# Kernel tuning notes

Measured on AMD Instinct MI355X. Metric: run time of the kernel, lower is better.

The kernel has to match this reference:

```python
import jax, jax.numpy as jnp
import numpy as np

N = 500000
C = 128
G = 4096


def setup_inputs() -> dict:
    key = jax.random.key(0)
    ks = jax.random.split(key, 6)
    x = jax.random.normal(ks[0], (N, C), dtype=jnp.float32)
    proj_w = jax.random.normal(ks[1], (C, C), dtype=jnp.float32) * (1.0 / np.sqrt(C))
    proj_b = jax.random.normal(ks[2], (C,), dtype=jnp.float32) * 0.01
    score_w = jax.random.normal(ks[3], (1, C), dtype=jnp.float32) * (1.0 / np.sqrt(C))
    score_b = jax.random.normal(ks[4], (1,), dtype=jnp.float32) * 0.01
    batch = jnp.sort(jax.random.randint(ks[5], (N,), 0, G, dtype=jnp.int32))
    return {"x": x, "proj_w": proj_w, "proj_b": proj_b,
            "score_w": score_w, "score_b": score_b,
            "batch": batch, "num_graphs": G}


def reference(x, proj_w, proj_b, score_w, score_b, batch, num_graphs):
    # h = tanh(Linear(x)); s = Linear(h) -> [N]
    h = jnp.tanh(x @ proj_w.T + proj_b)
    s = (h @ score_w.T + score_b)[:, 0]  # [N]
    # segment softmax over nodes of each graph
    m = jax.ops.segment_max(s, batch, num_segments=num_graphs)  # [G]
    m = jnp.where(jnp.isfinite(m), m, 0.0)  # guard empty segments
    e = jnp.exp(s - m[batch])
    denom = jax.ops.segment_sum(e, batch, num_segments=num_graphs)  # [G]
    w = e / jnp.maximum(denom[batch], 1e-30)  # [N]
    # weighted scatter-sum of raw features
    pooled = jax.ops.segment_sum(x * w[:, None], batch, num_segments=num_graphs)  # [G, C]
    return pooled
```

## Files before the change

### kernel.cpp

```cpp
#include <hip/hip_runtime.h>
#include <hip/hip_bf16.h>
#include <float.h>
#include <math.h>

#define CDIM 128

typedef __attribute__((ext_vector_type(8))) short short8v;
typedef __attribute__((ext_vector_type(4))) short short4v;
typedef __attribute__((ext_vector_type(4))) float f32x4;

__device__ __forceinline__ short bf16b(float f) {
    __hip_bfloat16 h = __float2bfloat16(f);
    return __builtin_bit_cast(short, h);
}

__device__ __forceinline__ float tanh_fast(float y) {
    float e = __expf(2.0f * y);
    return 1.0f - 2.0f / (e + 1.0f);
}

__device__ __forceinline__ int lower_bound_i(const int* __restrict__ b, int n, int v) {
    int lo = 0, hi = n;
    while (lo < hi) { int mid = (lo + hi) >> 1; if (b[mid] < v) lo = mid + 1; else hi = mid; }
    return lo;
}

__global__ void seg_bounds_kernel(const int* __restrict__ batch, int N, int G,
                                  int* __restrict__ seg) {
    int g = blockIdx.x * blockDim.x + threadIdx.x;
    if (g < G) seg[g] = lower_bound_i(batch, N, g);
    if (g == 0) seg[G] = N;
}

__global__ void wconv_kernel(const float* __restrict__ proj_w, short* __restrict__ wfrag) {
    int tid = blockIdx.x * 256 + threadIdx.x;
    int f = tid >> 6, l = tid & 63;
    int c  = ((f >> 2) << 4) | (l & 15);
    int k0 = ((f & 3) << 5) | ((l >> 4) << 3);
    short8v v;
    #pragma unroll
    for (int j = 0; j < 8; ++j) v[j] = bf16b(proj_w[c * CDIM + k0 + j]);
    ((short8v*)wfrag)[tid] = v;
}

__launch_bounds__(256, 4)
__global__ void pool_kernel(const float* __restrict__ x,
                            const short* __restrict__ wfrag,
                            const float* __restrict__ proj_b,
                            const float* __restrict__ score_w,
                            const float* __restrict__ score_b,
                            const int* __restrict__ seg,
                            float* __restrict__ out,
                            int N) {
    __shared__ short XsB[64 * 128];
    __shared__ float ps[4 * 64];
    __shared__ float cs[64];
    __shared__ __align__(16) float red[8 * 128];
    __shared__ float bc[2];

    const int g = blockIdx.x;
    const int t = threadIdx.x;
    const int lane = t & 63;
    const int w = t >> 6;
    const int start = seg[g];
    const int cnt = seg[g + 1] - start;

    if (cnt <= 0) {
        if (t < CDIM) out[g * CDIM + t] = 0.0f;
        return;
    }

    short8v wf[2][4];
    {
        const short8v* wfg = (const short8v*)wfrag;
        #pragma unroll
        for (int j = 0; j < 2; ++j)
            #pragma unroll
            for (int ks = 0; ks < 4; ++ks)
                wf[j][ks] = wfg[((((w << 1) | j) << 2 | ks) << 6) | lane];
    }
    float swl[2], pbl[2];
    #pragma unroll
    for (int j = 0; j < 2; ++j) {
        swl[j] = score_w[(((w << 1) | j) << 4) + (lane & 15)];
        pbl[j] = proj_b[(((w << 1) | j) << 4) + (lane & 15)];
    }
    const float sb = score_b[0];

    const float4* __restrict__ x4 = (const float4*)x;
    const int g8 = t >> 5;
    const int c4 = t & 31;
    const int al = lane & 15, ah = lane >> 4;

    float m_run = -FLT_MAX, l_run = 0.0f;
    float4 pa = make_float4(0.f, 0.f, 0.f, 0.f);

    for (int cb = 0; cb < cnt; cb += 64) {
        const int chunk_n = min(64, cnt - cb);

        float4 xr[8];
        #pragma unroll
        for (int i = 0; i < 8; ++i) {
            int row = g8 + (i << 3);
            size_t gr = (size_t)min(start + cb + row, N - 1);
            xr[i] = x4[gr * 32 + c4];
        }
        #pragma unroll
        for (int i = 0; i < 8; ++i) {
            int row = g8 + (i << 3);
            short4v b;
            b[0] = bf16b(xr[i].x); b[1] = bf16b(xr[i].y);
            b[2] = bf16b(xr[i].z); b[3] = bf16b(xr[i].w);
            *(short4v*)&XsB[(row << 7) | ((c4 << 2) ^ ((row & 7) << 3))] = b;
        }
        __syncthreads();

        #pragma unroll
        for (int rt = 0; rt < 4; ++rt) {
            const int arow = (rt << 4) | al;
            const int rsw = (arow & 7) << 3;
            f32x4 a0 = (f32x4){0.f, 0.f, 0.f, 0.f};
            f32x4 a1 = (f32x4){0.f, 0.f, 0.f, 0.f};
            #pragma unroll
            for (int ks = 0; ks < 4; ++ks) {
                short8v af = *(const short8v*)&XsB[(arow << 7) | (((ks << 5) | (ah << 3)) ^ rsw)];
                a0 = __builtin_amdgcn_mfma_f32_16x16x32_bf16(af, wf[0][ks], a0, 0, 0, 0);
                a1 = __builtin_amdgcn_mfma_f32_16x16x32_bf16(af, wf[1][ks], a1, 0, 0, 0);
            }
            #pragma unroll
            for (int r = 0; r < 4; ++r) {
                float s = swl[0] * tanh_fast(a0[r] + pbl[0])
                        + swl[1] * tanh_fast(a1[r] + pbl[1]);
                s += __shfl_xor(s, 1); s += __shfl_xor(s, 2);
                s += __shfl_xor(s, 4); s += __shfl_xor(s, 8);
                if (al == 0) ps[(w << 6) | (rt << 4) | (ah << 2) | r] = s;
            }
        }
        __syncthreads();

        if (t < 64) {
            float v = (t < chunk_n)
                    ? (ps[t] + ps[64 + t] + ps[128 + t] + ps[192 + t] + sb)
                    : -FLT_MAX;
            float mx = v;
            mx = fmaxf(mx, __shfl_xor(mx, 1));  mx = fmaxf(mx, __shfl_xor(mx, 2));
            mx = fmaxf(mx, __shfl_xor(mx, 4));  mx = fmaxf(mx, __shfl_xor(mx, 8));
            mx = fmaxf(mx, __shfl_xor(mx, 16)); mx = fmaxf(mx, __shfl_xor(mx, 32));
            float m_new = fmaxf(m_run, mx);
            float sc = __expf(m_run - m_new);
            float e = (t < chunk_n) ? __expf(v - m_new) : 0.f;
            float ssum = e;
            ssum += __shfl_xor(ssum, 1);  ssum += __shfl_xor(ssum, 2);
            ssum += __shfl_xor(ssum, 4);  ssum += __shfl_xor(ssum, 8);
            ssum += __shfl_xor(ssum, 16); ssum += __shfl_xor(ssum, 32);
            cs[t] = e;
            if (t == 0) { bc[0] = sc; bc[1] = ssum; }
            m_run = m_new;
        }
        __syncthreads();

        const float sc = bc[0];
        l_run = l_run * sc + bc[1];
        pa.x *= sc; pa.y *= sc; pa.z *= sc; pa.w *= sc;
        #pragma unroll
        for (int i = 0; i < 8; ++i) {
            float e = cs[g8 + (i << 3)];
            pa.x += e * xr[i].x; pa.y += e * xr[i].y;
            pa.z += e * xr[i].z; pa.w += e * xr[i].w;
        }
    }

    *(float4*)&red[(g8 << 7) + (c4 << 2)] = pa;
    __syncthreads();
    if (t < CDIM) {
        float v = 0.f;
        #pragma unroll
        for (int j = 0; j < 8; ++j) v += red[j * CDIM + t];
        out[g * CDIM + t] = v * (1.0f / fmaxf(l_run, 1e-30f));
    }
}

extern "C" void kernel_launch(void* const* d_in, const int* in_sizes, int n_in,
                              void* d_out, int out_size, void* d_ws, size_t ws_size,
                              hipStream_t stream) {
    const float* x       = (const float*)d_in[0];
    const float* proj_w  = (const float*)d_in[1];
    const float* proj_b  = (const float*)d_in[2];
    const float* score_w = (const float*)d_in[3];
    const float* score_b = (const float*)d_in[4];
    const int*   batch   = (const int*)d_in[5];

    const int N = in_sizes[0] / CDIM;
    const int G = out_size / CDIM;

    int*   seg   = (int*)d_ws;
    short* wfrag = (short*)((char*)d_ws + (((size_t)(G + 1) * 4 + 255) & ~(size_t)255));

    seg_bounds_kernel<<<(G + 255) / 256, 256, 0, stream>>>(batch, N, G, seg);
    wconv_kernel<<<8, 256, 0, stream>>>(proj_w, wfrag);
    pool_kernel<<<G, 256, 0, stream>>>(x, wfrag, proj_b, score_w, score_b,
                                       seg, (float*)d_out, N);
}
```

Before: 94.64 us.

## Assign one wavefront per graph with barrier-free online softmax pooling

Reworks the pooling kernel so that each wavefront processes one whole graph in 16-row chunks, and each block now holds four graphs. The projection weights are staged once per block in LDS, and the A fragments are built directly from registers, so the XsB shared tile is no longer used. The per-chunk softmax reduction and the final pooled reduction are now done with wave shuffles instead of block-wide __syncthreads, and the softmax rescale is skipped when the running max does not change. In exchange, the chunks are smaller (16 rows instead of 64), more accumulator registers are held per lane, and every block copies 32KB of weights into LDS, which may reduce occupancy.

```diff
diff --git a/kernel.cpp b/kernel.cpp
--- a/kernel.cpp
+++ b/kernel.cpp
@@ -6,7 +6,6 @@
 #define CDIM 128
 
 typedef __attribute__((ext_vector_type(8))) short short8v;
-typedef __attribute__((ext_vector_type(4))) short short4v;
 typedef __attribute__((ext_vector_type(4))) float f32x4;
 
 __device__ __forceinline__ short bf16b(float f) {
@@ -51,132 +50,140 @@
                             const float* __restrict__ score_b,
                             const int* __restrict__ seg,
                             float* __restrict__ out,
-                            int N) {
-    __shared__ short XsB[64 * 128];
-    __shared__ float ps[4 * 64];
-    __shared__ float cs[64];
-    __shared__ __align__(16) float red[8 * 128];
-    __shared__ float bc[2];
-
-    const int g = blockIdx.x;
+                            int N, int G) {
+    __shared__ short8v Wl[2048];
+    __shared__ float2  pbsw[128];
+
     const int t = threadIdx.x;
+    {
+        const short8v* wfg = (const short8v*)wfrag;
+        #pragma unroll
+        for (int i = 0; i < 8; ++i) Wl[t + (i << 8)] = wfg[t + (i << 8)];
+        if (t < 128) pbsw[t] = make_float2(proj_b[t], score_w[t]);
+    }
+    __syncthreads();
+
     const int lane = t & 63;
-    const int w = t >> 6;
+    const int g = (blockIdx.x << 2) | (t >> 6);
+    if (g >= G) return;
+    float* og = out + (size_t)g * CDIM;
+
     const int start = seg[g];
     const int cnt = seg[g + 1] - start;
-
     if (cnt <= 0) {
-        if (t < CDIM) out[g * CDIM + t] = 0.0f;
+        if (lane < 32) ((float4*)og)[lane] = make_float4(0.f, 0.f, 0.f, 0.f);
         return;
     }
 
-    short8v wf[2][4];
-    {
-        const short8v* wfg = (const short8v*)wfrag;
-        #pragma unroll
-        for (int j = 0; j < 2; ++j)
+    const int rl = lane & 15;
+    const int cg = lane >> 4;
+    const float sb = score_b[0];
+
+    float m_run = -FLT_MAX, l_run = 0.0f;
+    float4 pa[8];
+    #pragma unroll
+    for (int i = 0; i < 8; ++i) pa[i] = make_float4(0.f, 0.f, 0.f, 0.f);
+
+    for (int cb = 0; cb < cnt; cb += 16) {
+        const int rem = cnt - cb;
+
+        const int row = start + cb + min(rl, rem - 1);
+        const float4* xp = (const float4*)(x + (size_t)row * CDIM + (cg << 3));
+        float4 xr[8];
+        #pragma unroll
+        for (int ks = 0; ks < 4; ++ks) {
+            xr[ks * 2]     = xp[ks * 8];
+            xr[ks * 2 + 1] = xp[ks * 8 + 1];
+        }
+
+        short8v af[4];
+        #pragma unroll
+        for (int ks = 0; ks < 4; ++ks) {
+            float4 a = xr[ks * 2], b = xr[ks * 2 + 1];
+            af[ks][0] = bf16b(a.x); af[ks][1] = bf16b(a.y);
+            af[ks][2] = bf16b(a.z); af[ks][3] = bf16b(a.w);
+            af[ks][4] = bf16b(b.x); af[ks][5] = bf16b(b.y);
+            af[ks][6] = bf16b(b.z); af[ks][7] = bf16b(b.w);
+        }
+
+        float scp[4] = {0.f, 0.f, 0.f, 0.f};
+        #pragma unroll
+        for (int ct = 0; ct < 8; ++ct) {
+            f32x4 acc = (f32x4){0.f, 0.f, 0.f, 0.f};
             #pragma unroll
             for (int ks = 0; ks < 4; ++ks)
-                wf[j][ks] = wfg[((((w << 1) | j) << 2 | ks) << 6) | lane];
-    }
-    float swl[2], pbl[2];
+                acc = __builtin_amdgcn_mfma_f32_16x16x32_bf16(af[ks], Wl[(((ct << 2) | ks) << 6) | lane], acc, 0, 0, 0);
+            const float2 pb = pbsw[(ct << 4) | rl];
+            #pragma unroll
+            for (int r = 0; r < 4; ++r)
+                scp[r] += pb.y * tanh_fast(acc[r] + pb.x);
+        }
+
+        float sv[4]; float mx = -FLT_MAX;
+        #pragma unroll
+        for (int r = 0; r < 4; ++r) {
+            float v = scp[r];
+            v += __shfl_xor(v, 1); v += __shfl_xor(v, 2);
+            v += __shfl_xor(v, 4); v += __shfl_xor(v, 8);
+            sv[r] = ((cg << 2) + r < rem) ? (v + sb) : -FLT_MAX;
+            mx = fmaxf(mx, sv[r]);
+        }
+        mx = fmaxf(mx, __shfl_xor(mx, 16));
+        mx = fmaxf(mx, __shfl_xor(mx, 32));
+
+        const float m_new = fmaxf(m_run, mx);
+        float e_[4]; float ssum = 0.f;
+        #pragma unroll
+        for (int r = 0; r < 4; ++r) {
+            e_[r] = ((cg << 2) + r < rem) ? __expf(sv[r] - m_new) : 0.f;
+            ssum += e_[r];
+        }
+        ssum += __shfl_xor(ssum, 16);
+        ssum += __shfl_xor(ssum, 32);
+        if (mx > m_run) {
+            const float sc = __expf(m_run - m_new);
+            l_run *= sc;
+            #pragma unroll
+            for (int i = 0; i < 8; ++i) {
+                pa[i].x *= sc; pa[i].y *= sc; pa[i].z *= sc; pa[i].w *= sc;
+            }
+        }
+        m_run = m_new;
+        l_run += ssum;
+
+        const int src = (rl >> 2) << 4;
+        const float er0 = __shfl(e_[0], src), er1 = __shfl(e_[1], src);
+        const float er2 = __shfl(e_[2], src), er3 = __shfl(e_[3], src);
+        const int rr = rl & 3;
+        const float em = rr == 0 ? er0 : rr == 1 ? er1 : rr == 2 ? er2 : er3;
+
+        #pragma unroll
+        for (int i = 0; i < 8; ++i) {
+            pa[i].x += em * xr[i].x; pa[i].y += em * xr[i].y;
+            pa[i].z += em * xr[i].z; pa[i].w += em * xr[i].w;
+        }
+    }
+
     #pragma unroll
-    for (int j = 0; j < 2; ++j) {
-        swl[j] = score_w[(((w << 1) | j) << 4) + (lane & 15)];
-        pbl[j] = proj_b[(((w << 1) | j) << 4) + (lane & 15)];
-    }
-    const float sb = score_b[0];
-
-    const float4* __restrict__ x4 = (const float4*)x;
-    const int g8 = t >> 5;
-    const int c4 = t & 31;
-    const int al = lane & 15, ah = lane >> 4;
-
-    float m_run = -FLT_MAX, l_run = 0.0f;
-    float4 pa = make_float4(0.f, 0.f, 0.f, 0.f);
-
-    for (int cb = 0; cb < cnt; cb += 64) {
-        const int chunk_n = min(64, cnt - cb);
-
-        float4 xr[8];
+    for (int m = 1; m <= 8; m <<= 1) {
         #pragma unroll
         for (int i = 0; i < 8; ++i) {
-            int row = g8 + (i << 3);
-            size_t gr = (size_t)min(start + cb + row, N - 1);
-            xr[i] = x4[gr * 32 + c4];
-        }
-        #pragma unroll
-        for (int i = 0; i < 8; ++i) {
-            int row = g8 + (i << 3);
-            short4v b;
-            b[0] = bf16b(xr[i].x); b[1] = bf16b(xr[i].y);
-            b[2] = bf16b(xr[i].z); b[3] = bf16b(xr[i].w);
-            *(short4v*)&XsB[(row << 7) | ((c4 << 2) ^ ((row & 7) << 3))] = b;
-        }
-        __syncthreads();
-
-        #pragma unroll
-        for (int rt = 0; rt < 4; ++rt) {
-            const int arow = (rt << 4) | al;
-            const int rsw = (arow & 7) << 3;
-            f32x4 a0 = (f32x4){0.f, 0.f, 0.f, 0.f};
-            f32x4 a1 = (f32x4){0.f, 0.f, 0.f, 0.f};
-            #pragma unroll
-            for (int ks = 0; ks < 4; ++ks) {
-                short8v af = *(const short8v*)&XsB[(arow << 7) | (((ks << 5) | (ah << 3)) ^ rsw)];
-                a0 = __builtin_amdgcn_mfma_f32_16x16x32_bf16(af, wf[0][ks], a0, 0, 0, 0);
-                a1 = __builtin_amdgcn_mfma_f32_16x16x32_bf16(af, wf[1][ks], a1, 0, 0, 0);
+            pa[i].x += __shfl_xor(pa[i].x, m); pa[i].y += __shfl_xor(pa[i].y, m);
+            pa[i].z += __shfl_xor(pa[i].z, m); pa[i].w += __shfl_xor(pa[i].w, m);
+        }
+    }
+    const float inv = 1.0f / fmaxf(l_run, 1e-30f);
+    if (rl == 0) {
+        float4* o4 = (float4*)og;
+        #pragma unroll
+        for (int ks = 0; ks < 4; ++ks) {
+            #pragma unroll
+            for (int half = 0; half < 2; ++half) {
+                float4 v = pa[ks * 2 + half];
+                v.x *= inv; v.y *= inv; v.z *= inv; v.w *= inv;
+                o4[ks * 8 + half + (cg << 1)] = v;
             }
-            #pragma unroll
-            for (int r = 0; r < 4; ++r) {
-                float s = swl[0] * tanh_fast(a0[r] + pbl[0])
-                        + swl[1] * tanh_fast(a1[r] + pbl[1]);
-                s += __shfl_xor(s, 1); s += __shfl_xor(s, 2);
-                s += __shfl_xor(s, 4); s += __shfl_xor(s, 8);
-                if (al == 0) ps[(w << 6) | (rt << 4) | (ah << 2) | r] = s;
-            }
-        }
-        __syncthreads();
-
-        if (t < 64) {
-            float v = (t < chunk_n)
-                    ? (ps[t] + ps[64 + t] + ps[128 + t] + ps[192 + t] + sb)
-                    : -FLT_MAX;
-            float mx = v;
-            mx = fmaxf(mx, __shfl_xor(mx, 1));  mx = fmaxf(mx, __shfl_xor(mx, 2));
-            mx = fmaxf(mx, __shfl_xor(mx, 4));  mx = fmaxf(mx, __shfl_xor(mx, 8));
-            mx = fmaxf(mx, __shfl_xor(mx, 16)); mx = fmaxf(mx, __shfl_xor(mx, 32));
-            float m_new = fmaxf(m_run, mx);
-            float sc = __expf(m_run - m_new);
-            float e = (t < chunk_n) ? __expf(v - m_new) : 0.f;
-            float ssum = e;
-            ssum += __shfl_xor(ssum, 1);  ssum += __shfl_xor(ssum, 2);
-            ssum += __shfl_xor(ssum, 4);  ssum += __shfl_xor(ssum, 8);
-            ssum += __shfl_xor(ssum, 16); ssum += __shfl_xor(ssum, 32);
-            cs[t] = e;
-            if (t == 0) { bc[0] = sc; bc[1] = ssum; }
-            m_run = m_new;
-        }
-        __syncthreads();
-
-        const float sc = bc[0];
-        l_run = l_run * sc + bc[1];
-        pa.x *= sc; pa.y *= sc; pa.z *= sc; pa.w *= sc;
-        #pragma unroll
-        for (int i = 0; i < 8; ++i) {
-            float e = cs[g8 + (i << 3)];
-            pa.x += e * xr[i].x; pa.y += e * xr[i].y;
-            pa.z += e * xr[i].z; pa.w += e * xr[i].w;
-        }
-    }
-
-    *(float4*)&red[(g8 << 7) + (c4 << 2)] = pa;
-    __syncthreads();
-    if (t < CDIM) {
-        float v = 0.f;
-        #pragma unroll
-        for (int j = 0; j < 8; ++j) v += red[j * CDIM + t];
-        out[g * CDIM + t] = v * (1.0f / fmaxf(l_run, 1e-30f));
+        }
     }
 }
 
@@ -198,6 +205,6 @@
 
     seg_bounds_kernel<<<(G + 255) / 256, 256, 0, stream>>>(batch, N, G, seg);
     wconv_kernel<<<8, 256, 0, stream>>>(proj_w, wfrag);
-    pool_kernel<<<G, 256, 0, stream>>>(x, wfrag, proj_b, score_w, score_b,
-                                       seg, (float*)d_out, N);
-}
+    pool_kernel<<<(G + 3) / 4, 256, 0, stream>>>(x, wfrag, proj_b, score_w, score_b,
+                                                 seg, (float*)d_out, N, G);
+}
```

New measurement: 262.2 us. 2.77x slower.
